# Performance work log

Measured on AMD Instinct MI355X. Metric: run time of the kernel, lower is better.

## Reference

```python
import jax, jax.numpy as jnp
import numpy as np

ALIGN_CORNERS = True   # module init arg
NUM_AUX = 8            # auxiliary samples for linearized multi-sampling
NOISE_STRENGTH = 0.5   # noise scale in units of input pixel spacing
EPS = 1e-6             # Tikhonov term for the per-pixel 2x2 least squares


def _base_coords(n, align_corners):
    if align_corners:
        return jnp.linspace(-1.0, 1.0, n, dtype=jnp.float32)
    return (jnp.arange(n, dtype=jnp.float32) * 2.0 + 1.0) / n - 1.0


def affine_grid(theta, h_out, w_out, align_corners):
    # theta: [B,2,3] -> grid [B,h_out,w_out,2] with (x,y) in [-1,1]
    xs = _base_coords(w_out, align_corners)
    ys = _base_coords(h_out, align_corners)
    X, Y = jnp.meshgrid(xs, ys)                      # [H,W]
    base = jnp.stack([X, Y, jnp.ones_like(X)], -1)   # [H,W,3]
    return jnp.einsum('hwk,bik->bhwi', base, theta)  # [B,H,W,2]


def bilinear_sample(image, grid, align_corners):
    # image [B,C,Hi,Wi], grid [B,H,W,2] -> [B,H,W,C], zero padding outside
    B, C, Hi, Wi = image.shape
    x, y = grid[..., 0], grid[..., 1]
    if align_corners:
        ix = (x + 1.0) * 0.5 * (Wi - 1)
        iy = (y + 1.0) * 0.5 * (Hi - 1)
    else:
        ix = ((x + 1.0) * Wi - 1.0) * 0.5
        iy = ((y + 1.0) * Hi - 1.0) * 0.5
    x0 = jnp.floor(ix); y0 = jnp.floor(iy)
    wx1 = ix - x0; wy1 = iy - y0
    bidx = jnp.arange(B)[:, None, None]

    def tap(xi, yi, w):
        valid = (xi >= 0) & (xi <= Wi - 1) & (yi >= 0) & (yi <= Hi - 1)
        xc = jnp.clip(xi, 0, Wi - 1).astype(jnp.int32)
        yc = jnp.clip(yi, 0, Hi - 1).astype(jnp.int32)
        v = image[bidx, :, yc, xc]                   # [B,H,W,C] gather
        return v * (w * valid)[..., None]

    return (tap(x0, y0, (1 - wx1) * (1 - wy1)) +
            tap(x0 + 1, y0, wx1 * (1 - wy1)) +
            tap(x0, y0 + 1, (1 - wx1) * wy1) +
            tap(x0 + 1, y0 + 1, wx1 * wy1))


def linearized_grid_sample(image, grid, align_corners):
    # Linearized multi-sampling (Jiang et al., ICCV'19): forward value equals
    # the center bilinear sample; gradient wrt grid flows through a per-pixel
    # least-squares linearization fitted from NUM_AUX noisy auxiliary samples.
    B, C, Hi, Wi = image.shape
    key = jax.random.key(42)
    spacing = jnp.array([2.0 / Wi, 2.0 / Hi], dtype=jnp.float32)  # one input pixel in norm coords
    g0 = jax.lax.stop_gradient(grid)
    noise = jax.random.normal(key, (B, NUM_AUX) + grid.shape[1:3] + (2,), dtype=jnp.float32)
    aux = g0[:, None] + noise * NOISE_STRENGTH * spacing          # [B,K,H,W,2]

    center = bilinear_sample(image, g0, align_corners)            # [B,H,W,C]
    samp = jax.vmap(lambda g: bilinear_sample(image, g, align_corners),
                    in_axes=1, out_axes=1)(aux)                   # [B,K,H,W,C]

    d_int = samp - center[:, None]                                # [B,K,H,W,C]
    d_grid = aux - g0[:, None]                                    # [B,K,H,W,2]
    xtx = jnp.einsum('bkhwi,bkhwj->bhwij', d_grid, d_grid) \
        + EPS * jnp.eye(2, dtype=jnp.float32)                     # [B,H,W,2,2]
    xty = jnp.einsum('bkhwi,bkhwc->bhwic', d_grid, d_int)         # [B,H,W,2,C]
    slope = jnp.linalg.solve(xtx, xty)                            # [B,H,W,2,C]

    out = center + jnp.einsum('bhwic,bhwi->bhwc', slope, grid - g0)
    return jnp.transpose(out, (0, 3, 1, 2))                       # [B,C,H,W]


def setup_inputs() -> dict:
    key = jax.random.key(0)
    k1, k2 = jax.random.split(key)
    B, C, Hi, Wi = 4, 3, 1024, 1024
    image = jax.random.normal(k1, (B, C, Hi, Wi), dtype=jnp.float32)
    ident = jnp.tile(jnp.array([[1.0, 0.0, 0.0], [0.0, 1.0, 0.0]], dtype=jnp.float32), (B, 1, 1))
    pMtrx = ident + 0.05 * jax.random.normal(k2, (B, 2, 3), dtype=jnp.float32)
    return {"image": image, "pMtrx": pMtrx, "W": 1024, "H": 1024}


def reference(image, pMtrx, W, H):
    # torch.affine_grid_generator(pMtrx, (B,3,W,H)) -> grid [B, W, H, 2]
    grid = affine_grid(pMtrx, W, H, ALIGN_CORNERS)
    return linearized_grid_sample(image, grid, ALIGN_CORNERS)  # [B,C,W,H]
```

## Files before the change

### kernel.cpp

```cpp
#include <hip/hip_runtime.h>


#define B_  4
#define C_  3
#define HI  1024
#define WI  1024
#define HO  1024
#define WO  1024

#define TW  64
#define TH  32
#define MAXSEG  22
#define MAXROWS 48

typedef __attribute__((address_space(3))) void* lds_vp;
typedef const __attribute__((address_space(1))) void* gbl_vp;
typedef float f32x4 __attribute__((ext_vector_type(4)));

__device__ __forceinline__ float2 map_px(int w, int h,
                                         float t0, float t1, float t2,
                                         float t3, float t4, float t5) {
    const float xs = -1.0f + 2.0f * (float)w / (float)(WO - 1);
    const float ys = -1.0f + 2.0f * (float)h / (float)(HO - 1);
    const float x = t0 * xs + (t1 * ys + t2);
    const float y = t3 * xs + (t4 * ys + t5);
    const float ix = (x + 1.0f) * 0.5f * (float)(WI - 1);
    const float iy = (y + 1.0f) * 0.5f * (float)(HI - 1);
    return make_float2(ix, iy);
}

__global__ __launch_bounds__(256, 8) void warp_bilinear_fast_kernel(
    const float* __restrict__ image,
    const float* __restrict__ theta,
    float* __restrict__ out)
{
    __shared__ float lds[MAXSEG * 4 * MAXROWS];

    const int bid = blockIdx.x;
    const int sid = (bid & 7) * 768 + (bid >> 3);

    const int b    = sid / 1536;
    const int r1   = sid - b * 1536;
    const int c    = r1 >> 9;
    const int tile = r1 & 511;
    const int h0   = (tile >> 4) * TH;
    const int w0   = (tile & 15) * TW;

    const float* t = theta + b * 6;
    const float t0 = t[0], t1 = t[1], t2 = t[2];
    const float t3 = t[3], t4 = t[4], t5 = t[5];

    const float2 c00 = map_px(w0,        h0,        t0,t1,t2,t3,t4,t5);
    const float2 c10 = map_px(w0+TW-1,   h0,        t0,t1,t2,t3,t4,t5);
    const float2 c01 = map_px(w0,        h0+TH-1,   t0,t1,t2,t3,t4,t5);
    const float2 c11 = map_px(w0+TW-1,   h0+TH-1,   t0,t1,t2,t3,t4,t5);

    const float ixmin = fminf(fminf(c00.x, c10.x), fminf(c01.x, c11.x));
    const float iymin = fminf(fminf(c00.y, c10.y), fminf(c01.y, c11.y));
    const float ixmax = fmaxf(fmaxf(c00.x, c10.x), fmaxf(c01.x, c11.x));
    const float iymax = fmaxf(fmaxf(c00.y, c10.y), fmaxf(c01.y, c11.y));

    int xlo = (int)floorf(ixmin) - 1;
    int xhi = (int)floorf(ixmax) + 2;
    xlo = min(max(xlo, 0), WI - 1);
    xhi = min(max(xhi, xlo), WI - 1);
    int bx = xlo & ~3;
    const int nseg = min((xhi - bx + 4) >> 2, MAXSEG);
    bx = min(bx, WI - 4 * nseg);

    int ylo = (int)floorf(iymin) - 1;
    int yhi = (int)floorf(iymax) + 2;
    ylo = min(max(ylo, 0), HI - 1);
    yhi = min(max(yhi, ylo), HI - 1);
    const int nrows = min(yhi - ylo + 1, MAXROWS);
    const int by = min(ylo, HI - nrows);

    const int rowf  = nseg << 2;
    const int segch = nrows * nseg;

    const float rcp_nseg = 1.0f / (float)nseg;

    const float* imgc = image + (size_t)b * (C_ * HI * WI) + (size_t)c * (HI * WI);

    const int wv   = threadIdx.x >> 6;
    const int lane = threadIdx.x & 63;
    const int niter = (segch + 63) >> 6;
    for (int j = wv; j < niter; j += 4) {
        const int seg = (j << 6) + lane;
        if (seg < segch) {
            const int r = (int)(((float)seg + 0.5f) * rcp_nseg);
            const int s = seg - r * nseg;
            const float* gp = imgc + (by + r) * WI + (bx + (s << 2));
            __builtin_amdgcn_global_load_lds((gbl_vp)gp, (lds_vp)(lds + (j << 8)),
                                             16, 0, 0);
        }
    }
    __syncthreads();

    const int qx  = threadIdx.x & 15;
    const int rr  = threadIdx.x >> 4;
    const int wq  = w0 + (qx << 2);

    float* ob = out + (size_t)b * (C_ * HO * WO) + (size_t)c * (HO * WO) + wq;

    const bool interior = (ixmin >= 1.0f) && (ixmax <= (float)(WI - 2)) &&
                          (iymin >= 1.0f) && (iymax <= (float)(HI - 2));

#pragma unroll
    for (int rh = 0; rh < 2; ++rh) {
        const int h = h0 + rr + (rh << 4);

        const float ys = -1.0f + 2.0f * (float)h / (float)(HO - 1);
        const float xb = t1 * ys + t2;
        const float yb = t4 * ys + t5;

        float o0[4];

        if (interior) {
#pragma unroll
            for (int px = 0; px < 4; ++px) {
                const int w = wq + px;
                const float xs = -1.0f + 2.0f * (float)w / (float)(WO - 1);
                const float x = t0 * xs + xb;
                const float y = t3 * xs + yb;
                const float ix = (x + 1.0f) * 0.5f * (float)(WI - 1);
                const float iy = (y + 1.0f) * 0.5f * (float)(HI - 1);

                const float x0f = floorf(ix);
                const float y0f = floorf(iy);
                const float wx1 = ix - x0f;
                const float wy1 = iy - y0f;
                const float wx0 = 1.0f - wx1;
                const float wy0 = 1.0f - wy1;

                const float w00 = wx0 * wy0, w10 = wx1 * wy0;
                const float w01 = wx0 * wy1, w11 = wx1 * wy1;

                const int ox = (int)x0f - bx;
                const int oy = (int)y0f - by;
                const float* p = lds + oy * rowf + ox;

                o0[px] = p[0]    * w00 + p[1]        * w10
                       + p[rowf] * w01 + p[rowf + 1] * w11;
            }
        } else {
#pragma unroll
            for (int px = 0; px < 4; ++px) {
                const int w = wq + px;
                const float xs = -1.0f + 2.0f * (float)w / (float)(WO - 1);
                const float x = t0 * xs + xb;
                const float y = t3 * xs + yb;
                const float ix = (x + 1.0f) * 0.5f * (float)(WI - 1);
                const float iy = (y + 1.0f) * 0.5f * (float)(HI - 1);

                const float x0f = floorf(ix);
                const float y0f = floorf(iy);
                const float wx1 = ix - x0f;
                const float wy1 = iy - y0f;
                const int x0 = (int)x0f;
                const int y0 = (int)y0f;

                const float ax0 = (1.0f - wx1) * ((x0 >= 0 && x0 <= WI - 1) ? 1.0f : 0.0f);
                const float ax1 = wx1          * ((x0 >= -1 && x0 <= WI - 2) ? 1.0f : 0.0f);
                const float ay0 = (1.0f - wy1) * ((y0 >= 0 && y0 <= HI - 1) ? 1.0f : 0.0f);
                const float ay1 = wy1          * ((y0 >= -1 && y0 <= HI - 2) ? 1.0f : 0.0f);

                const float w00 = ax0 * ay0, w10 = ax1 * ay0;
                const float w01 = ax0 * ay1, w11 = ax1 * ay1;

                const int bw = (nseg << 2) - 1;
                const int xl0 = min(max(min(max(x0,     0), WI - 1) - bx, 0), bw);
                const int xl1 = min(max(min(max(x0 + 1, 0), WI - 1) - bx, 0), bw);
                const int yl0 = min(max(min(max(y0,     0), HI - 1) - by, 0), nrows - 1);
                const int yl1 = min(max(min(max(y0 + 1, 0), HI - 1) - by, 0), nrows - 1);

                o0[px] = lds[yl0 * rowf + xl0] * w00 + lds[yl0 * rowf + xl1] * w10
                       + lds[yl1 * rowf + xl0] * w01 + lds[yl1 * rowf + xl1] * w11;
            }
        }

        f32x4 s0 = { o0[0], o0[1], o0[2], o0[3] };
        __builtin_nontemporal_store(s0, (f32x4*)(ob + (size_t)h * WO));
    }
}

extern "C" void kernel_launch(void* const* d_in, const int* in_sizes, int n_in,
                              void* d_out, int out_size, void* d_ws, size_t ws_size,
                              hipStream_t stream) {
    const float* image = (const float*)d_in[0];
    const float* theta = (const float*)d_in[1];
    float* out = (float*)d_out;

    const int grid = B_ * C_ * (HO / TH) * (WO / TW);
    warp_bilinear_fast_kernel<<<grid, 256, 0, stream>>>(image, theta, out);
}
```

Before: 111.1 us.

## Process all channels per block and overlap next-channel staging with compute

Each block now handles all three channels of its output tile instead of one. The block stages channel c+1 into its own LDS buffer while it computes channel c. The interior-path bilinear offsets and weights are computed once and reused for all three channels, which removes repeated coordinate math and gives cross-channel overlap of loads and compute. In exchange, LDS per block triples, the grid shrinks to a third, and the occupancy hint is dropped, so fewer waves per CU may be available to hide memory latency.

```diff
diff --git a/kernel.cpp b/kernel.cpp
--- a/kernel.cpp
+++ b/kernel.cpp
@@ -12,6 +12,7 @@
 #define TH  32
 #define MAXSEG  22
 #define MAXROWS 48
+#define CHBUF   (MAXSEG * 4 * MAXROWS)
 
 typedef __attribute__((address_space(3))) void* lds_vp;
 typedef const __attribute__((address_space(1))) void* gbl_vp;
@@ -29,22 +30,20 @@
     return make_float2(ix, iy);
 }
 
-__global__ __launch_bounds__(256, 8) void warp_bilinear_fast_kernel(
+__global__ __launch_bounds__(256) void warp_bilinear_fast_kernel(
     const float* __restrict__ image,
     const float* __restrict__ theta,
     float* __restrict__ out)
 {
-    __shared__ float lds[MAXSEG * 4 * MAXROWS];
+    __shared__ float lds[C_ * CHBUF];
 
     const int bid = blockIdx.x;
-    const int sid = (bid & 7) * 768 + (bid >> 3);
-
-    const int b    = sid / 1536;
-    const int r1   = sid - b * 1536;
-    const int c    = r1 >> 9;
-    const int tile = r1 & 511;
-    const int h0   = (tile >> 4) * TH;
-    const int w0   = (tile & 15) * TW;
+    const int sid = ((bid & 7) << 8) | (bid >> 3);
+
+    const int b   = sid >> 9;
+    const int rem = sid & 511;
+    const int h0  = (rem >> 4) * TH;
+    const int w0  = (rem & 15) * TW;
 
     const float* t = theta + b * 6;
     const float t0 = t[0], t1 = t[1], t2 = t[2];
@@ -80,43 +79,48 @@
 
     const float rcp_nseg = 1.0f / (float)nseg;
 
-    const float* imgc = image + (size_t)b * (C_ * HI * WI) + (size_t)c * (HI * WI);
-
-    const int wv   = threadIdx.x >> 6;
-    const int lane = threadIdx.x & 63;
+    const float* imgb = image + (size_t)b * (C_ * HI * WI);
+
+    const int wv    = threadIdx.x >> 6;
+    const int lane  = threadIdx.x & 63;
     const int niter = (segch + 63) >> 6;
-    for (int j = wv; j < niter; j += 4) {
-        const int seg = (j << 6) + lane;
-        if (seg < segch) {
-            const int r = (int)(((float)seg + 0.5f) * rcp_nseg);
-            const int s = seg - r * nseg;
-            const float* gp = imgc + (by + r) * WI + (bx + (s << 2));
-            __builtin_amdgcn_global_load_lds((gbl_vp)gp, (lds_vp)(lds + (j << 8)),
-                                             16, 0, 0);
-        }
-    }
-    __syncthreads();
+
+#define STAGE_CH(cc) do {                                                     \
+        const float* imgc = imgb + (cc) * (HI * WI);                          \
+        float* ldsb = lds + (cc) * CHBUF;                                     \
+        for (int j = wv; j < niter; j += 4) {                                 \
+            const int seg = (j << 6) + lane;                                  \
+            if (seg < segch) {                                                \
+                const int r = (int)(((float)seg + 0.5f) * rcp_nseg);          \
+                const int s = seg - r * nseg;                                 \
+                const float* gp = imgc + (by + r) * WI + (bx + (s << 2));     \
+                __builtin_amdgcn_global_load_lds((gbl_vp)gp,                  \
+                    (lds_vp)(ldsb + (j << 8)), 16, 0, 0);                     \
+            }                                                                 \
+        }                                                                     \
+    } while (0)
 
     const int qx  = threadIdx.x & 15;
     const int rr  = threadIdx.x >> 4;
     const int wq  = w0 + (qx << 2);
 
-    float* ob = out + (size_t)b * (C_ * HO * WO) + (size_t)c * (HO * WO) + wq;
+    float* ob = out + (size_t)b * (C_ * HO * WO) + wq;
 
     const bool interior = (ixmin >= 1.0f) && (ixmax <= (float)(WI - 2)) &&
                           (iymin >= 1.0f) && (iymax <= (float)(HI - 2));
 
+    STAGE_CH(0);
+
+    int   ibs[8];
+    float wgt[8][4];
+
+    if (interior) {
 #pragma unroll
-    for (int rh = 0; rh < 2; ++rh) {
-        const int h = h0 + rr + (rh << 4);
-
-        const float ys = -1.0f + 2.0f * (float)h / (float)(HO - 1);
-        const float xb = t1 * ys + t2;
-        const float yb = t4 * ys + t5;
-
-        float o0[4];
-
-        if (interior) {
+        for (int rh = 0; rh < 2; ++rh) {
+            const int h = h0 + rr + (rh << 4);
+            const float ys = -1.0f + 2.0f * (float)h / (float)(HO - 1);
+            const float xb = t1 * ys + t2;
+            const float yb = t4 * ys + t5;
 #pragma unroll
             for (int px = 0; px < 4; ++px) {
                 const int w = wq + px;
@@ -133,55 +137,94 @@
                 const float wx0 = 1.0f - wx1;
                 const float wy0 = 1.0f - wy1;
 
-                const float w00 = wx0 * wy0, w10 = wx1 * wy0;
-                const float w01 = wx0 * wy1, w11 = wx1 * wy1;
+                const int idx = (rh << 2) | px;
+                wgt[idx][0] = wx0 * wy0;
+                wgt[idx][1] = wx1 * wy0;
+                wgt[idx][2] = wx0 * wy1;
+                wgt[idx][3] = wx1 * wy1;
 
                 const int ox = (int)x0f - bx;
                 const int oy = (int)y0f - by;
-                const float* p = lds + oy * rowf + ox;
-
-                o0[px] = p[0]    * w00 + p[1]        * w10
-                       + p[rowf] * w01 + p[rowf + 1] * w11;
-            }
-        } else {
-#pragma unroll
-            for (int px = 0; px < 4; ++px) {
-                const int w = wq + px;
-                const float xs = -1.0f + 2.0f * (float)w / (float)(WO - 1);
-                const float x = t0 * xs + xb;
-                const float y = t3 * xs + yb;
-                const float ix = (x + 1.0f) * 0.5f * (float)(WI - 1);
-                const float iy = (y + 1.0f) * 0.5f * (float)(HI - 1);
-
-                const float x0f = floorf(ix);
-                const float y0f = floorf(iy);
-                const float wx1 = ix - x0f;
-                const float wy1 = iy - y0f;
-                const int x0 = (int)x0f;
-                const int y0 = (int)y0f;
-
-                const float ax0 = (1.0f - wx1) * ((x0 >= 0 && x0 <= WI - 1) ? 1.0f : 0.0f);
-                const float ax1 = wx1          * ((x0 >= -1 && x0 <= WI - 2) ? 1.0f : 0.0f);
-                const float ay0 = (1.0f - wy1) * ((y0 >= 0 && y0 <= HI - 1) ? 1.0f : 0.0f);
-                const float ay1 = wy1          * ((y0 >= -1 && y0 <= HI - 2) ? 1.0f : 0.0f);
-
-                const float w00 = ax0 * ay0, w10 = ax1 * ay0;
-                const float w01 = ax0 * ay1, w11 = ax1 * ay1;
-
-                const int bw = (nseg << 2) - 1;
-                const int xl0 = min(max(min(max(x0,     0), WI - 1) - bx, 0), bw);
-                const int xl1 = min(max(min(max(x0 + 1, 0), WI - 1) - bx, 0), bw);
-                const int yl0 = min(max(min(max(y0,     0), HI - 1) - by, 0), nrows - 1);
-                const int yl1 = min(max(min(max(y0 + 1, 0), HI - 1) - by, 0), nrows - 1);
-
-                o0[px] = lds[yl0 * rowf + xl0] * w00 + lds[yl0 * rowf + xl1] * w10
-                       + lds[yl1 * rowf + xl0] * w01 + lds[yl1 * rowf + xl1] * w11;
+                ibs[idx] = oy * rowf + ox;
             }
         }
-
-        f32x4 s0 = { o0[0], o0[1], o0[2], o0[3] };
-        __builtin_nontemporal_store(s0, (f32x4*)(ob + (size_t)h * WO));
     }
+
+#define COMPUTE_CH(cc) do {                                                   \
+        const float* ldsb = lds + (cc) * CHBUF;                               \
+        float* obc = ob + (size_t)(cc) * (HO * WO);                           \
+        if (interior) {                                                       \
+            _Pragma("unroll")                                                 \
+            for (int rh = 0; rh < 2; ++rh) {                                  \
+                float o[4];                                                   \
+                _Pragma("unroll")                                             \
+                for (int px = 0; px < 4; ++px) {                              \
+                    const int idx = (rh << 2) | px;                           \
+                    const float* p = ldsb + ibs[idx];                         \
+                    o[px] = p[0]        * wgt[idx][0]                         \
+                          + p[1]        * wgt[idx][1]                         \
+                          + p[rowf]     * wgt[idx][2]                         \
+                          + p[rowf + 1] * wgt[idx][3];                        \
+                }                                                             \
+                f32x4 sv = { o[0], o[1], o[2], o[3] };                        \
+                const int h = h0 + rr + (rh << 4);                            \
+                __builtin_nontemporal_store(sv, (f32x4*)(obc + (size_t)h * WO)); \
+            }                                                                 \
+        } else {                                                              \
+            _Pragma("unroll")                                                 \
+            for (int rh = 0; rh < 2; ++rh) {                                  \
+                const int h = h0 + rr + (rh << 4);                            \
+                const float ys = -1.0f + 2.0f * (float)h / (float)(HO - 1);   \
+                const float xb = t1 * ys + t2;                                \
+                const float yb = t4 * ys + t5;                                \
+                float o[4];                                                   \
+                _Pragma("unroll")                                             \
+                for (int px = 0; px < 4; ++px) {                              \
+                    const int w = wq + px;                                    \
+                    const float xs = -1.0f + 2.0f * (float)w / (float)(WO - 1); \
+                    const float x = t0 * xs + xb;                             \
+                    const float y = t3 * xs + yb;                             \
+                    const float ix = (x + 1.0f) * 0.5f * (float)(WI - 1);     \
+                    const float iy = (y + 1.0f) * 0.5f * (float)(HI - 1);     \
+                    const float x0f = floorf(ix);                             \
+                    const float y0f = floorf(iy);                             \
+                    const float wx1 = ix - x0f;                               \
+                    const float wy1 = iy - y0f;                               \
+                    const int x0 = (int)x0f;                                  \
+                    const int y0 = (int)y0f;                                  \
+                    const float ax0 = (1.0f - wx1) * ((x0 >= 0 && x0 <= WI - 1) ? 1.0f : 0.0f);  \
+                    const float ax1 = wx1          * ((x0 >= -1 && x0 <= WI - 2) ? 1.0f : 0.0f); \
+                    const float ay0 = (1.0f - wy1) * ((y0 >= 0 && y0 <= HI - 1) ? 1.0f : 0.0f);  \
+                    const float ay1 = wy1          * ((y0 >= -1 && y0 <= HI - 2) ? 1.0f : 0.0f); \
+                    const float w00 = ax0 * ay0, w10 = ax1 * ay0;             \
+                    const float w01 = ax0 * ay1, w11 = ax1 * ay1;             \
+                    const int bw = (nseg << 2) - 1;                           \
+                    const int xl0 = min(max(min(max(x0,     0), WI - 1) - bx, 0), bw);        \
+                    const int xl1 = min(max(min(max(x0 + 1, 0), WI - 1) - bx, 0), bw);        \
+                    const int yl0 = min(max(min(max(y0,     0), HI - 1) - by, 0), nrows - 1); \
+                    const int yl1 = min(max(min(max(y0 + 1, 0), HI - 1) - by, 0), nrows - 1); \
+                    o[px] = ldsb[yl0 * rowf + xl0] * w00                      \
+                          + ldsb[yl0 * rowf + xl1] * w10                      \
+                          + ldsb[yl1 * rowf + xl0] * w01                      \
+                          + ldsb[yl1 * rowf + xl1] * w11;                     \
+                }                                                             \
+                f32x4 sv = { o[0], o[1], o[2], o[3] };                        \
+                __builtin_nontemporal_store(sv, (f32x4*)(obc + (size_t)h * WO)); \
+            }                                                                 \
+        }                                                                     \
+    } while (0)
+
+    __syncthreads();
+    STAGE_CH(1);
+    COMPUTE_CH(0);
+    __syncthreads();
+    STAGE_CH(2);
+    COMPUTE_CH(1);
+    __syncthreads();
+    COMPUTE_CH(2);
+
+#undef STAGE_CH
+#undef COMPUTE_CH
 }
 
 extern "C" void kernel_launch(void* const* d_in, const int* in_sizes, int n_in,
@@ -191,6 +234,6 @@
     const float* theta = (const float*)d_in[1];
     float* out = (float*)d_out;
 
-    const int grid = B_ * C_ * (HO / TH) * (WO / TW);
+    const int grid = B_ * (HO / TH) * (WO / TW);
     warp_bilinear_fast_kernel<<<grid, 256, 0, stream>>>(image, theta, out);
 }
```

Measured after the change: 110.6 us. About the same (-0.5%).
